# Kernel optimization log

Measured on AMD Instinct MI355X. Metric: run time of the kernel, lower is better.

## Reference

```python
import jax, jax.numpy as jnp
import numpy as np

S = 4096      # total packed tokens
B = 8         # number of variable-length segments
E = 1152      # embed_dim (SigLIP2 so400m)
H = 16        # num_heads
D = E // H    # head_dim = 72


def setup_inputs() -> dict:
    key = jax.random.key(0)
    ks = jax.random.split(key, 8)
    w_std = 0.02
    theta = jax.random.uniform(ks[1], (S, D), jnp.float32, 0.0, 2.0 * np.pi)
    return {
        "hidden_states": jax.random.normal(ks[0], (S, E), jnp.float32),
        "cu_seqlens": jnp.arange(B + 1, dtype=jnp.int32) * (S // B),
        "cos": jnp.cos(theta),
        "sin": jnp.sin(theta),
        "Wq": jax.random.normal(ks[2], (E, E), jnp.float32) * w_std,
        "bq": jnp.zeros((E,), jnp.float32),
        "Wk": jax.random.normal(ks[3], (E, E), jnp.float32) * w_std,
        "bk": jnp.zeros((E,), jnp.float32),
        "Wv": jax.random.normal(ks[4], (E, E), jnp.float32) * w_std,
        "bv": jnp.zeros((E,), jnp.float32),
        "Wo": jax.random.normal(ks[5], (E, E), jnp.float32) * w_std,
        "bo": jnp.zeros((E,), jnp.float32),
    }


def _rotate_half(x):
    x1, x2 = jnp.split(x, 2, axis=-1)
    return jnp.concatenate((-x2, x1), axis=-1)


def reference(hidden_states, cu_seqlens, cos, sin, Wq, bq, Wk, bk, Wv, bv, Wo, bo):
    seq_len = hidden_states.shape[0]
    scale = np.float32(D) ** -0.5
    # projections -> [S, H, D]
    q = (hidden_states @ Wq.T + bq).reshape(seq_len, H, D)
    k = (hidden_states @ Wk.T + bk).reshape(seq_len, H, D)
    v = (hidden_states @ Wv.T + bv).reshape(seq_len, H, D)
    # inline RoPE (apply_rotary_pos_emb_vision): cos/sin broadcast over heads
    c = cos[:, None, :]
    s = sin[:, None, :]
    q = q * c + _rotate_half(q) * s
    k = k * c + _rotate_half(k) * s
    # segment id per token from cu_seqlens; block-diagonal attention mask
    seg = jnp.searchsorted(cu_seqlens[1:], jnp.arange(seq_len, dtype=cu_seqlens.dtype), side="right")
    mask = seg[:, None] == seg[None, :]                     # [S, S]
    scores = jnp.einsum("shd,thd->hst", q, k) * scale       # [H, S, S]
    neg = jnp.finfo(scores.dtype).min
    scores = jnp.where(mask[None, :, :], scores, neg)
    probs = jax.nn.softmax(scores, axis=-1)
    attn = jnp.einsum("hst,thd->shd", probs, v).reshape(seq_len, E)
    return attn @ Wo.T + bo
```

## Files before the change

### kernel.cpp

```cpp
#include <hip/hip_runtime.h>
#include <float.h>

#define S_LEN 4096
#define E_DIM 1152
#define NH    16
#define HD    72
#define HD2   36
#define NQKV  3456

typedef __attribute__((ext_vector_type(4))) float f32x4;
typedef __attribute__((ext_vector_type(8))) _Float16 f16x8;

__device__ __forceinline__ unsigned short f2h(float f) {
    union { _Float16 h; unsigned short u; } c;
    c.h = (_Float16)f;
    return c.u;
}

__device__ __forceinline__ void gload_lds16(const unsigned short* g, unsigned short* l) {
    __builtin_amdgcn_global_load_lds(
        (const __attribute__((address_space(1))) unsigned int*)g,
        (__attribute__((address_space(3))) unsigned int*)l, 16, 0, 0);
}

__global__ __launch_bounds__(256)
void pack_f16(const float* __restrict__ hs, const float* __restrict__ wq,
              const float* __restrict__ wk, const float* __restrict__ wv,
              const float* __restrict__ wo,
              unsigned short* __restrict__ hs_h, unsigned short* __restrict__ wqkv_h,
              unsigned short* __restrict__ wo_h)
{
    const float* src; unsigned short* dst; int n4;
    const int WSZ = E_DIM * E_DIM;
    switch (blockIdx.z) {
        case 0: src = hs; dst = hs_h;             n4 = S_LEN * E_DIM / 4; break;
        case 1: src = wq; dst = wqkv_h;           n4 = WSZ / 4; break;
        case 2: src = wk; dst = wqkv_h + WSZ;     n4 = WSZ / 4; break;
        case 3: src = wv; dst = wqkv_h + 2 * WSZ; n4 = WSZ / 4; break;
        default: src = wo; dst = wo_h;            n4 = WSZ / 4; break;
    }
    for (int i = blockIdx.x * 256 + threadIdx.x; i < n4; i += gridDim.x * 256) {
        f32x4 x = ((const f32x4*)src)[i];
        ushort4 hv;
        hv.x = f2h(x[0]); hv.y = f2h(x[1]); hv.z = f2h(x[2]); hv.w = f2h(x[3]);
        ((ushort4*)dst)[i] = hv;
    }
}

__global__ __launch_bounds__(256, 4)
void gemm_qkv_f16(const unsigned short* __restrict__ Ah, const unsigned short* __restrict__ Wh,
                  const float* __restrict__ bq, const float* __restrict__ bk,
                  const float* __restrict__ bv,
                  float* __restrict__ oq, float* __restrict__ ok, float* __restrict__ ov)
{
    __shared__ unsigned short sA[128 * 32];
    __shared__ unsigned short sB[128 * 32];
    const int tid  = threadIdx.x;
    const int w    = tid >> 6, lane = tid & 63;
    const int quad = lane >> 4, m = lane & 15;
    const int wr   = w & 1,  wc = w >> 1;

    const int bid = blockIdx.x;
    const int lin = (bid & 7) * 108 + (bid >> 3);
    const int n_t = lin >> 5;
    const int m_t = lin & 31;
    const int m0  = m_t * 128;
    const int n0  = n_t * 128;

    const int srow = lane >> 2;
    const int skc  = (lane & 3) ^ ((lane >> 3) & 3);
    const size_t aoff0 = (size_t)(m0 + 32 * w + srow) * E_DIM + skc * 8;
    const size_t boff0 = (size_t)(n0 + 32 * w + srow) * E_DIM + skc * 8;

    f32x4 acc[4][4];
    #pragma unroll
    for (int i = 0; i < 4; ++i)
        #pragma unroll
        for (int j = 0; j < 4; ++j) acc[i][j] = (f32x4){0.f, 0.f, 0.f, 0.f};

    const int rsw = (m >> 1) & 3;

    for (int k0 = 0; k0 < E_DIM; k0 += 32) {
        #pragma unroll
        for (int c = 0; c < 2; ++c) {
            gload_lds16(Ah + aoff0 + (size_t)c * 16 * E_DIM + k0, &sA[(32 * w + 16 * c) * 32]);
            gload_lds16(Wh + boff0 + (size_t)c * 16 * E_DIM + k0, &sB[(32 * w + 16 * c) * 32]);
        }
        __syncthreads();

        f16x8 ah[4], bh[4];
        #pragma unroll
        for (int t = 0; t < 4; ++t) {
            ah[t] = *(const f16x8*)&sA[(64 * wr + 16 * t + m) * 32 + ((quad ^ rsw) * 8)];
            bh[t] = *(const f16x8*)&sB[(64 * wc + 16 * t + m) * 32 + ((quad ^ rsw) * 8)];
        }
        #pragma unroll
        for (int rt = 0; rt < 4; ++rt)
            #pragma unroll
            for (int ct = 0; ct < 4; ++ct)
                acc[rt][ct] = __builtin_amdgcn_mfma_f32_16x16x32_f16(ah[rt], bh[ct], acc[rt][ct], 0, 0, 0);
        __syncthreads();
    }

    const int which = n0 / E_DIM;
    const int n0l = n0 - which * E_DIM;
    const float* bp = (which == 0) ? bq : (which == 1) ? bk : bv;
    float* Cp       = (which == 0) ? oq : (which == 1) ? ok : ov;
    #pragma unroll
    for (int ct = 0; ct < 4; ++ct) {
        int col = n0l + 64 * wc + 16 * ct + m;
        float bias = bp[col];
        #pragma unroll
        for (int rt = 0; rt < 4; ++rt)
            #pragma unroll
            for (int reg = 0; reg < 4; ++reg) {
                int row = m0 + 64 * wr + 16 * rt + 4 * quad + reg;
                Cp[(size_t)row * E_DIM + col] = acc[rt][ct][reg] + bias;
            }
    }
}

__global__ __launch_bounds__(256, 3)
void gemm_out_f16(const unsigned short* __restrict__ Ah, const unsigned short* __restrict__ Wh,
                  const float* __restrict__ bo, float* __restrict__ Cp)
{
    __shared__ unsigned short sA[64 * 32];
    __shared__ unsigned short sB[128 * 32];
    const int tid  = threadIdx.x;
    const int w    = tid >> 6, lane = tid & 63;
    const int quad = lane >> 4, m = lane & 15;
    const int m0   = blockIdx.y * 64;
    const int n0   = blockIdx.x * 128;

    const int srow = lane >> 2;
    const int skc  = (lane & 3) ^ ((lane >> 3) & 3);
    const size_t aoff0 = (size_t)(m0 + 16 * w + srow) * E_DIM + skc * 8;
    const size_t boff0 = (size_t)(n0 + 32 * w + srow) * E_DIM + skc * 8;

    f32x4 acc[4][2];
    #pragma unroll
    for (int i = 0; i < 4; ++i)
        #pragma unroll
        for (int j = 0; j < 2; ++j) acc[i][j] = (f32x4){0.f, 0.f, 0.f, 0.f};

    const int rsw = (m >> 1) & 3;

    for (int k0 = 0; k0 < E_DIM; k0 += 32) {
        gload_lds16(Ah + aoff0 + k0, &sA[(16 * w) * 32]);
        #pragma unroll
        for (int c = 0; c < 2; ++c)
            gload_lds16(Wh + boff0 + (size_t)c * 16 * E_DIM + k0, &sB[(32 * w + 16 * c) * 32]);
        __syncthreads();
        f16x8 ah[4], bh[2];
        #pragma unroll
        for (int t = 0; t < 4; ++t)
            ah[t] = *(const f16x8*)&sA[(16 * t + m) * 32 + ((quad ^ rsw) * 8)];
        #pragma unroll
        for (int ct = 0; ct < 2; ++ct)
            bh[ct] = *(const f16x8*)&sB[(32 * w + 16 * ct + m) * 32 + ((quad ^ rsw) * 8)];
        #pragma unroll
        for (int rt = 0; rt < 4; ++rt)
            #pragma unroll
            for (int ct = 0; ct < 2; ++ct)
                acc[rt][ct] = __builtin_amdgcn_mfma_f32_16x16x32_f16(ah[rt], bh[ct], acc[rt][ct], 0, 0, 0);
        __syncthreads();
    }

    #pragma unroll
    for (int ct = 0; ct < 2; ++ct) {
        int col = n0 + 32 * w + 16 * ct + m;
        float bias = bo[col];
        #pragma unroll
        for (int rt = 0; rt < 4; ++rt)
            #pragma unroll
            for (int reg = 0; reg < 4; ++reg) {
                int row = m0 + 16 * rt + 4 * quad + reg;
                Cp[(size_t)row * E_DIM + col] = acc[rt][ct][reg] + bias;
            }
    }
}

__global__ __launch_bounds__(256)
void rope_pack(const float* __restrict__ q, const float* __restrict__ k,
               const float* __restrict__ cosb, const float* __restrict__ sinb,
               unsigned short* __restrict__ qb, unsigned short* __restrict__ kb)
{
    const float* x = (blockIdx.z == 0) ? q : k;
    unsigned short* ob = (blockIdx.z == 0) ? qb : kb;
    const int h = blockIdx.y;
    const int s0 = blockIdx.x * 32;
    for (int task = threadIdx.x; task < 32 * 18; task += 256) {
        int sl = task / 18, c = task % 18;
        int s = s0 + sl;
        int d0 = c << 2;
        const float* xr = x + (size_t)s * E_DIM + h * HD;
        f32x4 xa = *(const f32x4*)(xr + d0);
        f32x4 cc = *(const f32x4*)(cosb + (size_t)s * HD + d0);
        f32x4 sn = *(const f32x4*)(sinb + (size_t)s * HD + d0);
        f32x4 xp = *(const f32x4*)(xr + (d0 < HD2 ? d0 + HD2 : d0 - HD2));
        f32x4 r = (d0 < HD2) ? (xa * cc - xp * sn) : (xa * cc + xp * sn);
        unsigned int lo = (unsigned int)f2h(r[0]) | ((unsigned int)f2h(r[1]) << 16);
        unsigned int hi = (unsigned int)f2h(r[2]) | ((unsigned int)f2h(r[3]) << 16);
        unsigned int* dst = (unsigned int*)(ob + ((size_t)h * S_LEN + s) * HD + d0);
        dst[0] = lo; dst[1] = hi;
    }
}

__global__ __launch_bounds__(256)
void vtrans(const float* __restrict__ v, unsigned short* __restrict__ vt)
{
    __shared__ unsigned short tile[HD][72];
    const int h = blockIdx.y;
    const int s0 = blockIdx.x * 64;
    for (int task = threadIdx.x; task < 64 * 18; task += 256) {
        int r = task / 18, c = task % 18;
        f32x4 x = *(const f32x4*)(v + (size_t)(s0 + r) * E_DIM + h * HD + (c << 2));
        tile[(c << 2) + 0][r] = f2h(x[0]);
        tile[(c << 2) + 1][r] = f2h(x[1]);
        tile[(c << 2) + 2][r] = f2h(x[2]);
        tile[(c << 2) + 3][r] = f2h(x[3]);
    }
    __syncthreads();
    for (int task = threadIdx.x; task < HD * 8; task += 256) {
        int d = task / 8, cc = task % 8;
        uint4 val = *(const uint4*)&tile[d][cc << 3];
        *(uint4*)(vt + ((size_t)h * HD + d) * S_LEN + s0 + (cc << 3)) = val;
    }
}

__global__ __launch_bounds__(256, 4)
void attn_mfma(const unsigned short* __restrict__ qb, const unsigned short* __restrict__ kb,
               const unsigned short* __restrict__ vt, const int* __restrict__ cu,
               int nseg, unsigned short* __restrict__ out)
{
    __shared__ unsigned short ks_s[64][72];
    __shared__ unsigned short vs_s[80][72];
    __shared__ unsigned short ss_s[64][72];

    const int tid  = threadIdx.x;
    const int w    = tid >> 6;
    const int lane = tid & 63;
    const int quad = lane >> 4;
    const int m    = lane & 15;
    const int h    = blockIdx.y;
    const int qb0  = blockIdx.x * 64;
    const float scale = 0.11785113019775793f;

    {
        uint4 zz = make_uint4(0u, 0u, 0u, 0u);
        if (tid < 72) {
            int r = 72 + tid / 9, c = tid % 9;
            *(uint4*)&vs_s[r][c << 3] = zz;
        }
    }

    int rs_r[4], re_r[4];
    #pragma unroll
    for (int reg = 0; reg < 4; ++reg) {
        int row = qb0 + 16 * w + 4 * quad + reg;
        int st = 0;
        for (int i = 1; i < nseg; ++i) if (cu[i] <= row) st = i;
        rs_r[reg] = cu[st];
        re_r[reg] = cu[st + 1];
    }
    int st0 = 0, st1 = 0;
    for (int i = 1; i < nseg; ++i) {
        if (cu[i] <= qb0) st0 = i;
        if (cu[i] <= qb0 + 63) st1 = i;
    }
    const int kstart = cu[st0];
    const int kend   = cu[st1 + 1];

    f16x8 qf[3];
    {
        const unsigned short* qrow = qb + ((size_t)h * S_LEN + qb0 + 16 * w + m) * HD;
        #pragma unroll
        for (int k3 = 0; k3 < 3; ++k3) {
            bool pad = (k3 == 2) && (quad != 0);
            int off = pad ? 0 : (k3 * 32 + quad * 8);
            f16x8 val = *(const f16x8*)(qrow + off);
            f16x8 z = {0, 0, 0, 0, 0, 0, 0, 0};
            qf[k3] = pad ? z : val;
        }
    }

    f32x4 acc_o[5];
    #pragma unroll
    for (int i = 0; i < 5; ++i) acc_o[i] = (f32x4){0.f, 0.f, 0.f, 0.f};
    float l_r[4] = {0.f, 0.f, 0.f, 0.f};

    for (int kb_i = kstart; kb_i < kend; kb_i += 64) {
        __syncthreads();
        for (int slot = tid; slot < 64 * 9; slot += 256) {
            int r = slot / 9, c = slot % 9;
            int krow = kb_i + r; if (krow >= kend) krow = kend - 1;
            uint4 val = *(const uint4*)(kb + ((size_t)h * S_LEN + krow) * HD + (c << 3));
            *(uint4*)&ks_s[r][c << 3] = val;
        }
        for (int slot = tid; slot < 72 * 8; slot += 256) {
            int d = slot / 8, c = slot % 8;
            int kk0 = kb_i + (c << 3);
            if (kk0 > S_LEN - 8) kk0 = S_LEN - 8;
            uint4 val = *(const uint4*)(vt + ((size_t)h * HD + d) * S_LEN + kk0);
            *(uint4*)&vs_s[d][c << 3] = val;
        }
        __syncthreads();

        f32x4 sacc[4];
        #pragma unroll
        for (int ct = 0; ct < 4; ++ct) sacc[ct] = (f32x4){0.f, 0.f, 0.f, 0.f};
        #pragma unroll
        for (int ct = 0; ct < 4; ++ct) {
            const unsigned short* krow = &ks_s[16 * ct + m][0];
            #pragma unroll
            for (int k3 = 0; k3 < 3; ++k3) {
                bool pad = (k3 == 2) && (quad != 0);
                int off = pad ? 0 : (k3 * 32 + quad * 8);
                f16x8 bfr = *(const f16x8*)(krow + off);
                f16x8 z = {0, 0, 0, 0, 0, 0, 0, 0};
                bfr = pad ? z : bfr;
                sacc[ct] = __builtin_amdgcn_mfma_f32_16x16x32_f16(qf[k3], bfr, sacc[ct], 0, 0, 0);
            }
        }

        #pragma unroll
        for (int ct = 0; ct < 4; ++ct) {
            int key = kb_i + 16 * ct + m;
            #pragma unroll
            for (int reg = 0; reg < 4; ++reg) {
                bool valid = (key >= rs_r[reg]) && (key < re_r[reg]);
                float p = valid ? __expf(sacc[ct][reg] * scale) : 0.f;
                l_r[reg] += p;
                ss_s[16 * w + 4 * quad + reg][16 * ct + m] = f2h(p);
            }
        }

        {
            const unsigned short* prow = &ss_s[16 * w + m][0];
            f16x8 pf0 = *(const f16x8*)(prow + quad * 8);
            f16x8 pf1 = *(const f16x8*)(prow + 32 + quad * 8);
            #pragma unroll
            for (int ct2 = 0; ct2 < 5; ++ct2) {
                const unsigned short* vrow = &vs_s[16 * ct2 + m][0];
                f16x8 vf0 = *(const f16x8*)(vrow + quad * 8);
                f16x8 vf1 = *(const f16x8*)(vrow + 32 + quad * 8);
                acc_o[ct2] = __builtin_amdgcn_mfma_f32_16x16x32_f16(pf0, vf0, acc_o[ct2], 0, 0, 0);
                acc_o[ct2] = __builtin_amdgcn_mfma_f32_16x16x32_f16(pf1, vf1, acc_o[ct2], 0, 0, 0);
            }
        }
    }

    #pragma unroll
    for (int reg = 0; reg < 4; ++reg) {
        float l = l_r[reg];
        l += __shfl_xor(l, 1);
        l += __shfl_xor(l, 2);
        l += __shfl_xor(l, 4);
        l += __shfl_xor(l, 8);
        l_r[reg] = l;
    }

    #pragma unroll
    for (int reg = 0; reg < 4; ++reg) {
        float linv = (l_r[reg] > 0.f) ? 1.f / l_r[reg] : 0.f;
        int row = qb0 + 16 * w + 4 * quad + reg;
        unsigned short* orow = out + (size_t)row * E_DIM + h * HD;
        #pragma unroll
        for (int ct2 = 0; ct2 < 5; ++ct2) {
            int col = 16 * ct2 + m;
            if (col < HD) orow[col] = f2h(acc_o[ct2][reg] * linv);
        }
    }
}

extern "C" void kernel_launch(void* const* d_in, const int* in_sizes, int n_in,
                              void* d_out, int out_size, void* d_ws, size_t ws_size,
                              hipStream_t stream)
{
    const float* hs   = (const float*)d_in[0];
    const int*   cu   = (const int*)d_in[1];
    const float* cosb = (const float*)d_in[2];
    const float* sinb = (const float*)d_in[3];
    const float* Wq   = (const float*)d_in[4];
    const float* bq   = (const float*)d_in[5];
    const float* Wk   = (const float*)d_in[6];
    const float* bk   = (const float*)d_in[7];
    const float* Wv   = (const float*)d_in[8];
    const float* bv   = (const float*)d_in[9];
    const float* Wo   = (const float*)d_in[10];
    const float* bo   = (const float*)d_in[11];
    float* outp = (float*)d_out;

    const size_t mat = (size_t)S_LEN * E_DIM;
    float* qf = (float*)d_ws;
    float* kf = qf + mat;
    float* vf = kf + mat;
    unsigned short* hs_h   = (unsigned short*)(vf + mat);
    unsigned short* wqkv_h = hs_h + mat;
    unsigned short* wo_h   = wqkv_h + (size_t)NQKV * E_DIM;
    unsigned short* qbb     = hs_h;
    unsigned short* kbb     = hs_h + (size_t)NH * S_LEN * HD;
    unsigned short* kbb2   = wo_h + (size_t)E_DIM * E_DIM;
    unsigned short* vtb    = kbb2 + (size_t)NH * S_LEN * HD;
    unsigned short* attn_h = (unsigned short*)qf;

    const int nseg = in_sizes[1] - 1;

    dim3 gpack(512, 1, 5);
    pack_f16<<<gpack, 256, 0, stream>>>(hs, Wq, Wk, Wv, Wo, hs_h, wqkv_h, wo_h);

    gemm_qkv_f16<<<dim3(864), 256, 0, stream>>>(hs_h, wqkv_h, bq, bk, bv, qf, kf, vf);

    dim3 grope(S_LEN / 32, NH, 2);
    rope_pack<<<grope, 256, 0, stream>>>(qf, kf, cosb, sinb, qbb, kbb2);

    dim3 gvt(S_LEN / 64, NH, 1);
    vtrans<<<gvt, 256, 0, stream>>>(vf, vtb);

    dim3 gattn(S_LEN / 64, NH, 1);
    attn_mfma<<<gattn, 256, 0, stream>>>(qbb, kbb2, vtb, cu, nseg, attn_h);

    dim3 gout(E_DIM / 128, S_LEN / 64, 1);
    gemm_out_f16<<<gout, 256, 0, stream>>>(attn_h, wo_h, bo, outp);
}
```

Before: 230.8 us.

## Fuse RoPE into attention and widen GEMM K-tiles to 64

Removes the separate rope_pack kernel. The attention kernel now loads fp32 Q/K, applies rotary embedding on the fly and converts to fp16 in shared memory, which saves one launch and an intermediate fp16 round trip. The cost is that K is re-rotated from fp32 for every query tile, so K traffic and ALU work per tile grow. Both GEMMs also move from 32- to 64-wide K tiles with a new XOR swizzle, halving barrier count per K step at the cost of more LDS use.

```diff
diff --git a/kernel.cpp b/kernel.cpp
--- a/kernel.cpp
+++ b/kernel.cpp
@@ -53,8 +53,8 @@
                   const float* __restrict__ bv,
                   float* __restrict__ oq, float* __restrict__ ok, float* __restrict__ ov)
 {
-    __shared__ unsigned short sA[128 * 32];
-    __shared__ unsigned short sB[128 * 32];
+    __shared__ unsigned short sA[128 * 64];
+    __shared__ unsigned short sB[128 * 64];
     const int tid  = threadIdx.x;
     const int w    = tid >> 6, lane = tid & 63;
     const int quad = lane >> 4, m = lane & 15;
@@ -67,10 +67,8 @@
     const int m0  = m_t * 128;
     const int n0  = n_t * 128;
 
-    const int srow = lane >> 2;
-    const int skc  = (lane & 3) ^ ((lane >> 3) & 3);
-    const size_t aoff0 = (size_t)(m0 + 32 * w + srow) * E_DIM + skc * 8;
-    const size_t boff0 = (size_t)(n0 + 32 * w + srow) * E_DIM + skc * 8;
+    const int srow = lane >> 3;
+    const int skc  = (lane & 7) ^ srow;
 
     f32x4 acc[4][4];
     #pragma unroll
@@ -78,27 +76,32 @@
         #pragma unroll
         for (int j = 0; j < 4; ++j) acc[i][j] = (f32x4){0.f, 0.f, 0.f, 0.f};
 
-    const int rsw = (m >> 1) & 3;
-
-    for (int k0 = 0; k0 < E_DIM; k0 += 32) {
-        #pragma unroll
-        for (int c = 0; c < 2; ++c) {
-            gload_lds16(Ah + aoff0 + (size_t)c * 16 * E_DIM + k0, &sA[(32 * w + 16 * c) * 32]);
-            gload_lds16(Wh + boff0 + (size_t)c * 16 * E_DIM + k0, &sB[(32 * w + 16 * c) * 32]);
-        }
-        __syncthreads();
-
-        f16x8 ah[4], bh[4];
-        #pragma unroll
-        for (int t = 0; t < 4; ++t) {
-            ah[t] = *(const f16x8*)&sA[(64 * wr + 16 * t + m) * 32 + ((quad ^ rsw) * 8)];
-            bh[t] = *(const f16x8*)&sB[(64 * wc + 16 * t + m) * 32 + ((quad ^ rsw) * 8)];
-        }
-        #pragma unroll
-        for (int rt = 0; rt < 4; ++rt)
-            #pragma unroll
-            for (int ct = 0; ct < 4; ++ct)
-                acc[rt][ct] = __builtin_amdgcn_mfma_f32_16x16x32_f16(ah[rt], bh[ct], acc[rt][ct], 0, 0, 0);
+    const int rm7 = m & 7;
+
+    for (int k0 = 0; k0 < E_DIM; k0 += 64) {
+        #pragma unroll
+        for (int c = 0; c < 4; ++c) {
+            int r = 32 * w + 8 * c + srow;
+            gload_lds16(Ah + (size_t)(m0 + r) * E_DIM + k0 + skc * 8, &sA[(32 * w + 8 * c) * 64]);
+            gload_lds16(Wh + (size_t)(n0 + r) * E_DIM + k0 + skc * 8, &sB[(32 * w + 8 * c) * 64]);
+        }
+        __syncthreads();
+
+        #pragma unroll
+        for (int k3 = 0; k3 < 2; ++k3) {
+            f16x8 ah[4], bh[4];
+            #pragma unroll
+            for (int t = 0; t < 4; ++t) {
+                int pc = ((k3 << 2) + quad) ^ rm7;
+                ah[t] = *(const f16x8*)&sA[(64 * wr + 16 * t + m) * 64 + pc * 8];
+                bh[t] = *(const f16x8*)&sB[(64 * wc + 16 * t + m) * 64 + pc * 8];
+            }
+            #pragma unroll
+            for (int rt = 0; rt < 4; ++rt)
+                #pragma unroll
+                for (int ct = 0; ct < 4; ++ct)
+                    acc[rt][ct] = __builtin_amdgcn_mfma_f32_16x16x32_f16(ah[rt], bh[ct], acc[rt][ct], 0, 0, 0);
+        }
         __syncthreads();
     }
 
@@ -120,22 +123,20 @@
     }
 }
 
-__global__ __launch_bounds__(256, 3)
+__global__ __launch_bounds__(256, 4)
 void gemm_out_f16(const unsigned short* __restrict__ Ah, const unsigned short* __restrict__ Wh,
                   const float* __restrict__ bo, float* __restrict__ Cp)
 {
-    __shared__ unsigned short sA[64 * 32];
-    __shared__ unsigned short sB[128 * 32];
+    __shared__ unsigned short sA[64 * 64];
+    __shared__ unsigned short sB[128 * 64];
     const int tid  = threadIdx.x;
     const int w    = tid >> 6, lane = tid & 63;
     const int quad = lane >> 4, m = lane & 15;
     const int m0   = blockIdx.y * 64;
     const int n0   = blockIdx.x * 128;
 
-    const int srow = lane >> 2;
-    const int skc  = (lane & 3) ^ ((lane >> 3) & 3);
-    const size_t aoff0 = (size_t)(m0 + 16 * w + srow) * E_DIM + skc * 8;
-    const size_t boff0 = (size_t)(n0 + 32 * w + srow) * E_DIM + skc * 8;
+    const int srow = lane >> 3;
+    const int skc  = (lane & 7) ^ srow;
 
     f32x4 acc[4][2];
     #pragma unroll
@@ -143,26 +144,36 @@
         #pragma unroll
         for (int j = 0; j < 2; ++j) acc[i][j] = (f32x4){0.f, 0.f, 0.f, 0.f};
 
-    const int rsw = (m >> 1) & 3;
-
-    for (int k0 = 0; k0 < E_DIM; k0 += 32) {
-        gload_lds16(Ah + aoff0 + k0, &sA[(16 * w) * 32]);
-        #pragma unroll
-        for (int c = 0; c < 2; ++c)
-            gload_lds16(Wh + boff0 + (size_t)c * 16 * E_DIM + k0, &sB[(32 * w + 16 * c) * 32]);
-        __syncthreads();
-        f16x8 ah[4], bh[2];
-        #pragma unroll
-        for (int t = 0; t < 4; ++t)
-            ah[t] = *(const f16x8*)&sA[(16 * t + m) * 32 + ((quad ^ rsw) * 8)];
-        #pragma unroll
-        for (int ct = 0; ct < 2; ++ct)
-            bh[ct] = *(const f16x8*)&sB[(32 * w + 16 * ct + m) * 32 + ((quad ^ rsw) * 8)];
-        #pragma unroll
-        for (int rt = 0; rt < 4; ++rt)
+    const int rm7 = m & 7;
+
+    for (int k0 = 0; k0 < E_DIM; k0 += 64) {
+        #pragma unroll
+        for (int c = 0; c < 2; ++c) {
+            int r = 16 * w + 8 * c + srow;
+            gload_lds16(Ah + (size_t)(m0 + r) * E_DIM + k0 + skc * 8, &sA[(16 * w + 8 * c) * 64]);
+        }
+        #pragma unroll
+        for (int c = 0; c < 4; ++c) {
+            int r = 32 * w + 8 * c + srow;
+            gload_lds16(Wh + (size_t)(n0 + r) * E_DIM + k0 + skc * 8, &sB[(32 * w + 8 * c) * 64]);
+        }
+        __syncthreads();
+        #pragma unroll
+        for (int k3 = 0; k3 < 2; ++k3) {
+            f16x8 ah[4], bh[2];
+            int pc = ((k3 << 2) + quad) ^ rm7;
+            #pragma unroll
+            for (int t = 0; t < 4; ++t)
+                ah[t] = *(const f16x8*)&sA[(16 * t + m) * 64 + pc * 8];
             #pragma unroll
             for (int ct = 0; ct < 2; ++ct)
-                acc[rt][ct] = __builtin_amdgcn_mfma_f32_16x16x32_f16(ah[rt], bh[ct], acc[rt][ct], 0, 0, 0);
+                bh[ct] = *(const f16x8*)&sB[(32 * w + 16 * ct + m) * 64 + pc * 8];
+            #pragma unroll
+            for (int rt = 0; rt < 4; ++rt)
+                #pragma unroll
+                for (int ct = 0; ct < 2; ++ct)
+                    acc[rt][ct] = __builtin_amdgcn_mfma_f32_16x16x32_f16(ah[rt], bh[ct], acc[rt][ct], 0, 0, 0);
+        }
         __syncthreads();
     }
 
@@ -177,32 +188,6 @@
                 int row = m0 + 16 * rt + 4 * quad + reg;
                 Cp[(size_t)row * E_DIM + col] = acc[rt][ct][reg] + bias;
             }
-    }
-}
-
-__global__ __launch_bounds__(256)
-void rope_pack(const float* __restrict__ q, const float* __restrict__ k,
-               const float* __restrict__ cosb, const float* __restrict__ sinb,
-               unsigned short* __restrict__ qb, unsigned short* __restrict__ kb)
-{
-    const float* x = (blockIdx.z == 0) ? q : k;
-    unsigned short* ob = (blockIdx.z == 0) ? qb : kb;
-    const int h = blockIdx.y;
-    const int s0 = blockIdx.x * 32;
-    for (int task = threadIdx.x; task < 32 * 18; task += 256) {
-        int sl = task / 18, c = task % 18;
-        int s = s0 + sl;
-        int d0 = c << 2;
-        const float* xr = x + (size_t)s * E_DIM + h * HD;
-        f32x4 xa = *(const f32x4*)(xr + d0);
-        f32x4 cc = *(const f32x4*)(cosb + (size_t)s * HD + d0);
-        f32x4 sn = *(const f32x4*)(sinb + (size_t)s * HD + d0);
-        f32x4 xp = *(const f32x4*)(xr + (d0 < HD2 ? d0 + HD2 : d0 - HD2));
-        f32x4 r = (d0 < HD2) ? (xa * cc - xp * sn) : (xa * cc + xp * sn);
-        unsigned int lo = (unsigned int)f2h(r[0]) | ((unsigned int)f2h(r[1]) << 16);
-        unsigned int hi = (unsigned int)f2h(r[2]) | ((unsigned int)f2h(r[3]) << 16);
-        unsigned int* dst = (unsigned int*)(ob + ((size_t)h * S_LEN + s) * HD + d0);
-        dst[0] = lo; dst[1] = hi;
     }
 }
 
@@ -229,7 +214,8 @@
 }
 
 __global__ __launch_bounds__(256, 4)
-void attn_mfma(const unsigned short* __restrict__ qb, const unsigned short* __restrict__ kb,
+void attn_rope(const float* __restrict__ qf, const float* __restrict__ kf,
+               const float* __restrict__ cosb, const float* __restrict__ sinb,
                const unsigned short* __restrict__ vt, const int* __restrict__ cu,
                int nseg, unsigned short* __restrict__ out)
 {
@@ -271,16 +257,38 @@
     const int kstart = cu[st0];
     const int kend   = cu[st1 + 1];
 
-    f16x8 qf[3];
+    for (int task = tid; task < 64 * 9; task += 256) {
+        int row = task / 9, d0 = (task % 9) << 2;
+        int s = qb0 + row;
+        const float* xr = qf + (size_t)s * E_DIM + h * HD;
+        f32x4 a  = *(const f32x4*)(xr + d0);
+        f32x4 b  = *(const f32x4*)(xr + d0 + HD2);
+        f32x4 c1 = *(const f32x4*)(cosb + (size_t)s * HD + d0);
+        f32x4 s1 = *(const f32x4*)(sinb + (size_t)s * HD + d0);
+        f32x4 c2 = *(const f32x4*)(cosb + (size_t)s * HD + d0 + HD2);
+        f32x4 s2 = *(const f32x4*)(sinb + (size_t)s * HD + d0 + HD2);
+        f32x4 r1 = a * c1 - b * s1;
+        f32x4 r2 = b * c2 + a * s2;
+        uint2 u1, u2;
+        u1.x = (unsigned)f2h(r1[0]) | ((unsigned)f2h(r1[1]) << 16);
+        u1.y = (unsigned)f2h(r1[2]) | ((unsigned)f2h(r1[3]) << 16);
+        u2.x = (unsigned)f2h(r2[0]) | ((unsigned)f2h(r2[1]) << 16);
+        u2.y = (unsigned)f2h(r2[2]) | ((unsigned)f2h(r2[3]) << 16);
+        *(uint2*)&ks_s[row][d0]       = u1;
+        *(uint2*)&ks_s[row][d0 + HD2] = u2;
+    }
+    __syncthreads();
+
+    f16x8 qfr[3];
     {
-        const unsigned short* qrow = qb + ((size_t)h * S_LEN + qb0 + 16 * w + m) * HD;
+        const unsigned short* qrow = &ks_s[16 * w + m][0];
         #pragma unroll
         for (int k3 = 0; k3 < 3; ++k3) {
             bool pad = (k3 == 2) && (quad != 0);
             int off = pad ? 0 : (k3 * 32 + quad * 8);
             f16x8 val = *(const f16x8*)(qrow + off);
             f16x8 z = {0, 0, 0, 0, 0, 0, 0, 0};
-            qf[k3] = pad ? z : val;
+            qfr[k3] = pad ? z : val;
         }
     }
 
@@ -291,11 +299,25 @@
 
     for (int kb_i = kstart; kb_i < kend; kb_i += 64) {
         __syncthreads();
-        for (int slot = tid; slot < 64 * 9; slot += 256) {
-            int r = slot / 9, c = slot % 9;
-            int krow = kb_i + r; if (krow >= kend) krow = kend - 1;
-            uint4 val = *(const uint4*)(kb + ((size_t)h * S_LEN + krow) * HD + (c << 3));
-            *(uint4*)&ks_s[r][c << 3] = val;
+        for (int task = tid; task < 64 * 9; task += 256) {
+            int row = task / 9, d0 = (task % 9) << 2;
+            int s = kb_i + row; if (s >= kend) s = kend - 1;
+            const float* xr = kf + (size_t)s * E_DIM + h * HD;
+            f32x4 a  = *(const f32x4*)(xr + d0);
+            f32x4 b  = *(const f32x4*)(xr + d0 + HD2);
+            f32x4 c1 = *(const f32x4*)(cosb + (size_t)s * HD + d0);
+            f32x4 s1 = *(const f32x4*)(sinb + (size_t)s * HD + d0);
+            f32x4 c2 = *(const f32x4*)(cosb + (size_t)s * HD + d0 + HD2);
+            f32x4 s2 = *(const f32x4*)(sinb + (size_t)s * HD + d0 + HD2);
+            f32x4 r1 = a * c1 - b * s1;
+            f32x4 r2 = b * c2 + a * s2;
+            uint2 u1, u2;
+            u1.x = (unsigned)f2h(r1[0]) | ((unsigned)f2h(r1[1]) << 16);
+            u1.y = (unsigned)f2h(r1[2]) | ((unsigned)f2h(r1[3]) << 16);
+            u2.x = (unsigned)f2h(r2[0]) | ((unsigned)f2h(r2[1]) << 16);
+            u2.y = (unsigned)f2h(r2[2]) | ((unsigned)f2h(r2[3]) << 16);
+            *(uint2*)&ks_s[row][d0]       = u1;
+            *(uint2*)&ks_s[row][d0 + HD2] = u2;
         }
         for (int slot = tid; slot < 72 * 8; slot += 256) {
             int d = slot / 8, c = slot % 8;
@@ -319,7 +341,7 @@
                 f16x8 bfr = *(const f16x8*)(krow + off);
                 f16x8 z = {0, 0, 0, 0, 0, 0, 0, 0};
                 bfr = pad ? z : bfr;
-                sacc[ct] = __builtin_amdgcn_mfma_f32_16x16x32_f16(qf[k3], bfr, sacc[ct], 0, 0, 0);
+                sacc[ct] = __builtin_amdgcn_mfma_f32_16x16x32_f16(qfr[k3], bfr, sacc[ct], 0, 0, 0);
             }
         }
 
@@ -398,11 +420,8 @@
     unsigned short* hs_h   = (unsigned short*)(vf + mat);
     unsigned short* wqkv_h = hs_h + mat;
     unsigned short* wo_h   = wqkv_h + (size_t)NQKV * E_DIM;
-    unsigned short* qbb     = hs_h;
-    unsigned short* kbb     = hs_h + (size_t)NH * S_LEN * HD;
-    unsigned short* kbb2   = wo_h + (size_t)E_DIM * E_DIM;
-    unsigned short* vtb    = kbb2 + (size_t)NH * S_LEN * HD;
-    unsigned short* attn_h = (unsigned short*)qf;
+    unsigned short* vtb    = wo_h + (size_t)E_DIM * E_DIM;
+    unsigned short* attn_h = hs_h;
 
     const int nseg = in_sizes[1] - 1;
 
@@ -411,14 +430,11 @@
 
     gemm_qkv_f16<<<dim3(864), 256, 0, stream>>>(hs_h, wqkv_h, bq, bk, bv, qf, kf, vf);
 
-    dim3 grope(S_LEN / 32, NH, 2);
-    rope_pack<<<grope, 256, 0, stream>>>(qf, kf, cosb, sinb, qbb, kbb2);
-
     dim3 gvt(S_LEN / 64, NH, 1);
     vtrans<<<gvt, 256, 0, stream>>>(vf, vtb);
 
     dim3 gattn(S_LEN / 64, NH, 1);
-    attn_mfma<<<gattn, 256, 0, stream>>>(qbb, kbb2, vtb, cu, nseg, attn_h);
+    attn_rope<<<gattn, 256, 0, stream>>>(qf, kf, cosb, sinb, vtb, cu, nseg, attn_h);
 
     dim3 gout(E_DIM / 128, S_LEN / 64, 1);
     gemm_out_f16<<<gout, 256, 0, stream>>>(attn_h, wo_h, bo, outp);
```

Result: faster. 224.3 us (-2.8%).
